# Kernel tuning notes

Hardware: AMD Instinct MI355X
Metric: run time of the kernel (lower is better)

The kernel has to match this reference:

```python
import jax, jax.numpy as jnp
import numpy as np

N = 5000      # nodes
E = 80000     # edges (avg degree 16)
B = 8         # batch of graph signals sharing one graph
IN = 30       # input feature dim (10 steps x 3)
H = 4         # attention heads
D = 64        # hidden dim per head
HD = H * D    # 256
OUT = 3       # output features per step
NUM_GAT_LAYERS = 4  # num_layer=5 -> 1 + (5-2) layers
EPS = 1e-5


def setup_inputs() -> dict:
    key = jax.random.key(0)
    ks = jax.random.split(key, 40)
    inp = {}
    inp["xx"] = jax.random.normal(ks[0], (B, N, IN), dtype=jnp.float32)
    inp["src"] = jax.random.randint(ks[1], (E,), 0, N, dtype=jnp.int32)
    inp["dst"] = jax.random.randint(ks[2], (E,), 0, N, dtype=jnp.int32)
    dims = [IN, HD, HD, HD]
    k = 3
    for l in range(NUM_GAT_LAYERS):
        fan_in = dims[l]
        inp[f"W{l}"] = jax.random.normal(ks[k], (fan_in, HD), dtype=jnp.float32) / np.sqrt(fan_in); k += 1
        inp[f"al{l}"] = jax.random.normal(ks[k], (H, D), dtype=jnp.float32) * 0.1; k += 1
        inp[f"ar{l}"] = jax.random.normal(ks[k], (H, D), dtype=jnp.float32) * 0.1; k += 1
        inp[f"gamma{l}"] = jnp.ones((HD,), dtype=jnp.float32)
        inp[f"beta{l}"] = jnp.zeros((HD,), dtype=jnp.float32)
    inp["W_out"] = jax.random.normal(ks[k], (HD, OUT), dtype=jnp.float32) / np.sqrt(HD); k += 1
    inp["b_out"] = jnp.zeros((OUT,), dtype=jnp.float32)
    inp["output_length"] = 5
    return inp


def _gat_conv(x, W, al, ar, src, dst):
    # DGL GATConv: fc -> per-head attn logits -> edge softmax over dst -> scatter-sum
    h = (x @ W).reshape(N, H, D)                       # [N,H,D]
    el = (h * al).sum(-1)                              # [N,H]
    er = (h * ar).sum(-1)                              # [N,H]
    e = jax.nn.leaky_relu(el[src] + er[dst], 0.2)      # [E,H]
    m = jax.ops.segment_max(e, dst, num_segments=N)    # [N,H] (stable softmax)
    ex = jnp.exp(e - m[dst])                           # [E,H]
    s = jax.ops.segment_sum(ex, dst, num_segments=N)   # [N,H]
    alpha = ex / s[dst]                                # [E,H]
    return jax.ops.segment_sum(alpha[:, :, None] * h[src], dst, num_segments=N)  # [N,H,D]


def _gat_layer(x, W, al, ar, gamma, beta, src, dst):
    # per-sample GATConv, flatten heads, BatchNorm1d (training stats) over (B,N), LeakyReLU
    out = jax.vmap(lambda xb: _gat_conv(xb, W, al, ar, src, dst))(x)  # [B,N,H,D]
    out = out.reshape(B, N, HD)
    mu = out.mean(axis=(0, 1))
    var = out.var(axis=(0, 1))  # biased, matches torch BN normalization
    out = (out - mu) * jax.lax.rsqrt(var + EPS) * gamma + beta
    return jax.nn.leaky_relu(out, 0.01)


def reference(xx, src, dst,
              W0, al0, ar0, gamma0, beta0,
              W1, al1, ar1, gamma1, beta1,
              W2, al2, ar2, gamma2, beta2,
              W3, al3, ar3, gamma3, beta3,
              W_out, b_out, output_length):
    layers = [(W0, al0, ar0, gamma0, beta0),
              (W1, al1, ar1, gamma1, beta1),
              (W2, al2, ar2, gamma2, beta2),
              (W3, al3, ar3, gamma3, beta3)]
    outputs = []
    for _ in range(output_length):
        h = xx
        for (W, al, ar, g, b) in layers:
            h = _gat_layer(h, W, al, ar, g, b, src, dst)
        out = h @ W_out + b_out                      # [B,N,OUT]
        xx = jnp.concatenate([xx[:, :, 3:], out], axis=-1)
        outputs.append(out[:, :, None, :])
    return jnp.concatenate(outputs, axis=2)          # [B,N,T,OUT]
```

## Files before the change

### kernel.cpp

```cpp
#include <hip/hip_runtime.h>
#include <math.h>

#define NNODES 5000
#define NEDGES 80000
#define NB 8
#define NIN 30
#define K0PAD 32
#define NH 4
#define ND 64
#define NHD 256
#define NT 5
#define NOUT 3
#define ROWS (NB * NNODES)
#define BNEPS 1e-5f
#define KP 40
#define NREP 8
#define BM 32

#define GLOBAL_AS __attribute__((address_space(1)))
#define LDS_AS __attribute__((address_space(3)))

typedef short shortx8 __attribute__((ext_vector_type(8)));
typedef _Float16 halfx8 __attribute__((ext_vector_type(8)));
typedef _Float16 halfx4 __attribute__((ext_vector_type(4)));
typedef _Float16 halfx2 __attribute__((ext_vector_type(2)));
typedef float floatx4 __attribute__((ext_vector_type(4)));

static __device__ __forceinline__ unsigned short f2h(float f) {
    union { _Float16 h; unsigned short u; } v;
    v.h = (_Float16)f;
    return v.u;
}
static __device__ __forceinline__ float h2f(unsigned short u) {
    union { _Float16 h; unsigned short u; } v;
    v.u = u;
    return (float)v.h;
}


__global__ void count_kernel(const int* __restrict__ dst, int* __restrict__ counts, int n) {
    int e = blockIdx.x * blockDim.x + threadIdx.x;
    if (e < n) atomicAdd(&counts[dst[e]], 1);
}

__global__ __launch_bounds__(1024) void scan_kernel(const int* __restrict__ counts,
                                                    int* __restrict__ offsets, int n) {
    __shared__ int smem[1024];
    const int CH = 5;
    int tid = threadIdx.x;
    int base = tid * CH;
    int loc[CH];
    int s = 0;
    for (int j = 0; j < CH; ++j) {
        int i = base + j;
        int v = (i < n) ? counts[i] : 0;
        loc[j] = s;
        s += v;
    }
    smem[tid] = s;
    __syncthreads();
    for (int off = 1; off < 1024; off <<= 1) {
        int v = (tid >= off) ? smem[tid - off] : 0;
        __syncthreads();
        smem[tid] += v;
        __syncthreads();
    }
    int excl = smem[tid] - s;
    for (int j = 0; j < CH; ++j) {
        int i = base + j;
        if (i < n) offsets[i] = excl + loc[j];
    }
    if (tid == 1023) offsets[n] = smem[1023];
}

__global__ void fill_kernel(const int* __restrict__ src, const int* __restrict__ dst,
                            const int* __restrict__ offsets, int* __restrict__ cursor,
                            int* __restrict__ csr_src, int n) {
    int e = blockIdx.x * blockDim.x + threadIdx.x;
    if (e >= n) return;
    int d = dst[e];
    int pos = offsets[d] + atomicAdd(&cursor[d], 1);
    csr_src[pos] = src[e];
}


__global__ void pack_xx_kernel(const float* __restrict__ xx, unsigned short* __restrict__ xx16) {
    int idx = blockIdx.x * blockDim.x + threadIdx.x;
    if (idx >= ROWS * K0PAD) return;
    int g = idx >> 5;
    int k = idx & 31;
    float v = (k < NIN) ? xx[(size_t)g * NIN + k] : 0.0f;
    xx16[idx] = f2h(v);
}

__global__ void packWt_kernel(const float* __restrict__ W0, const float* __restrict__ W1,
                              const float* __restrict__ W2, const float* __restrict__ W3,
                              unsigned short* __restrict__ P0, unsigned short* __restrict__ P1,
                              unsigned short* __restrict__ P2, unsigned short* __restrict__ P3) {
    int l = blockIdx.y;
    const float* W = (l == 0) ? W0 : (l == 1) ? W1 : (l == 2) ? W2 : W3;
    unsigned short* WtP = (l == 0) ? P0 : (l == 1) ? P1 : (l == 2) ? P2 : P3;
    int Kin = (l == 0) ? NIN : NHD;
    int Kpad = (l == 0) ? K0PAD : NHD;
    int n = blockIdx.x;
    int k = threadIdx.x;
    if (k < Kpad) {
        float v = (k < Kin) ? W[(size_t)k * NHD + n] : 0.0f;
        int t = k >> 5;
        int quad = (k >> 3) & 3;
        int j = k & 7;
        int p = n * 4 + (quad ^ ((n >> 1) & 3));
        WtP[(size_t)t * (NHD * 32) + p * 8 + j] = f2h(v);
    }
}


__global__ __launch_bounds__(256) void gemm_mfma_kernel(
    const unsigned short* __restrict__ A, const unsigned short* __restrict__ Wt,
    const float* __restrict__ alw, const float* __restrict__ arw,
    const float* __restrict__ sums, const float* __restrict__ gamma,
    const float* __restrict__ beta, int apply_bn,
    unsigned short* __restrict__ C16, float* __restrict__ el, float* __restrict__ er,
    int K) {
    __shared__ __align__(16) short As[BM * KP];
    __shared__ __align__(16) short Bs[256 * 32];
    __shared__ float bn_scale[NHD];
    __shared__ float bn_shift[NHD];
    int tid = threadIdx.x;
    if (apply_bn) {
        int c = tid;
        float s = 0.0f, s2 = 0.0f;
#pragma unroll
        for (int r2 = 0; r2 < NREP; ++r2) {
            s += sums[r2 * 2 * NHD + c];
            s2 += sums[r2 * 2 * NHD + NHD + c];
        }
        const float invn = 1.0f / (float)ROWS;
        float mu = s * invn;
        float var = s2 * invn - mu * mu;
        float sc = rsqrtf(var + BNEPS) * gamma[c];
        bn_scale[c] = sc;
        bn_shift[c] = beta[c] - mu * sc;
    }
    __syncthreads();

    int wave = tid >> 6;
    int lane = tid & 63;
    int c = lane & 15;
    int quad = lane >> 4;
    int xorv = (c >> 1) & 3;
    int row0 = blockIdx.x * BM;

    floatx4 acc[2][4];
#pragma unroll
    for (int mt = 0; mt < 2; ++mt)
#pragma unroll
        for (int nt = 0; nt < 4; ++nt) acc[mt][nt] = (floatx4){0.f, 0.f, 0.f, 0.f};

    int r = tid >> 2;
    int seg = tid & 3;
    for (int k0 = 0; k0 < K; k0 += 32) {
        const unsigned short* gB = Wt + (size_t)(k0 >> 5) * (NHD * 32);
#pragma unroll
        for (int i = 0; i < 4; ++i) {
            int ci = i * 256 + tid;
            __builtin_amdgcn_global_load_lds(
                (const GLOBAL_AS unsigned int*)(gB + ci * 8),
                (LDS_AS unsigned int*)(&Bs[ci * 8]), 16, 0, 0);
        }
        if (r < BM) {
            shortx8 v = *(const shortx8*)(A + (size_t)(row0 + r) * K + k0 + seg * 8);
            if (apply_bn) {
                halfx8 hv = *(halfx8*)&v;
                int kg = k0 + seg * 8;
#pragma unroll
                for (int j = 0; j < 8; ++j) {
                    float x = (float)hv[j];
                    x = fmaf(x, bn_scale[kg + j], bn_shift[kg + j]);
                    x = (x > 0.0f) ? x : 0.01f * x;
                    hv[j] = (_Float16)x;
                }
                v = *(shortx8*)&hv;
            }
            *(shortx8*)(&As[r * KP + seg * 8]) = v;
        }
        __syncthreads();
        halfx8 a[2], b[4];
#pragma unroll
        for (int mt = 0; mt < 2; ++mt)
            a[mt] = *(const halfx8*)(&As[(mt * 16 + c) * KP + quad * 8]);
#pragma unroll
        for (int nt = 0; nt < 4; ++nt) {
            int pq = (wave * 64 + nt * 16 + c) * 4 + (quad ^ xorv);
            b[nt] = *(const halfx8*)(&Bs[pq * 8]);
        }
#pragma unroll
        for (int mt = 0; mt < 2; ++mt)
#pragma unroll
            for (int nt = 0; nt < 4; ++nt)
                acc[mt][nt] = __builtin_amdgcn_mfma_f32_16x16x32_f16(a[mt], b[nt],
                                                                     acc[mt][nt], 0, 0, 0);
        __syncthreads();
    }

    float alv[4], arv[4];
#pragma unroll
    for (int nt = 0; nt < 4; ++nt) {
        alv[nt] = alw[wave * 64 + nt * 16 + c];
        arv[nt] = arw[wave * 64 + nt * 16 + c];
    }
#pragma unroll
    for (int mt = 0; mt < 2; ++mt) {
#pragma unroll
        for (int rr = 0; rr < 4; ++rr) {
            int row = row0 + mt * 16 + quad * 4 + rr;
            float pl = 0.0f, pr = 0.0f;
#pragma unroll
            for (int nt = 0; nt < 4; ++nt) {
                float v = acc[mt][nt][rr];
                C16[(size_t)row * NHD + wave * 64 + nt * 16 + c] = f2h(v);
                pl += v * alv[nt];
                pr += v * arv[nt];
            }
#pragma unroll
            for (int o = 1; o < 16; o <<= 1) {
                pl += __shfl_xor(pl, o);
                pr += __shfl_xor(pr, o);
            }
            if (c == mt * 4 + rr) {
                el[(size_t)row * NH + wave] = pl;
                er[(size_t)row * NH + wave] = pr;
            }
        }
    }
}


__global__ __launch_bounds__(256) void attn_kernel(const unsigned short* __restrict__ h16,
                                                   const float* __restrict__ el,
                                                   const float* __restrict__ er,
                                                   const int* __restrict__ offsets,
                                                   const int* __restrict__ csr_src,
                                                   unsigned short* __restrict__ out16,
                                                   float* __restrict__ sums) {
    int p = blockIdx.x;
    int tid = threadIdx.x;
    if (p == 0) {
        for (int i = tid; i < NREP * 2 * NHD; i += 256) sums[i] = 0.0f;
    }
    int b = p & 7;
    int wave = tid >> 6;
    int lane = tid & 63;
    int head = lane >> 4;
    int li = lane & 15;
    int n = ((p >> 3) << 2) + wave;
    int g = b * NNODES + n;
    int start = offsets[n];
    int deg = offsets[n + 1] - start;
    if (deg == 0) {
        *(unsigned long long*)(out16 + (size_t)g * NHD + lane * 4) = 0ULL;
        return;
    }
    const float* elb = el + (size_t)b * NNODES * NH;
    float er_nh = er[(size_t)g * NH + head];

    if (deg <= 64) {
        float e[4], w[4];
        int s[4];
#pragma unroll
        for (int k = 0; k < 4; ++k) {
            int idx = k * 16 + li;
            if (idx < deg) {
                s[k] = csr_src[start + idx];
                float t = elb[s[k] * NH + head] + er_nh;
                e[k] = (t > 0.0f) ? t : 0.2f * t;
            } else {
                s[k] = 0;
                e[k] = -INFINITY;
            }
        }
        float mx = fmaxf(fmaxf(e[0], e[1]), fmaxf(e[2], e[3]));
#pragma unroll
        for (int o = 8; o; o >>= 1) mx = fmaxf(mx, __shfl_xor(mx, o));
        float sm = 0.0f;
#pragma unroll
        for (int k = 0; k < 4; ++k) {
            w[k] = __expf(e[k] - mx);
            sm += w[k];
        }
#pragma unroll
        for (int o = 8; o; o >>= 1) sm += __shfl_xor(sm, o);

        int sub = lane >> 5;
        int i32 = lane & 31;
        int hsel = (lane & 24) << 1;
        float smh = __shfl(sm, hsel);
        const unsigned short* hrow = h16 + (size_t)b * NNODES * NHD + i32 * 8;
        float a0 = 0.f, a1 = 0.f, a2 = 0.f, a3 = 0.f;
        float a4 = 0.f, a5 = 0.f, a6 = 0.f, a7 = 0.f;
#define GATHER_CHUNK(K)                                                          \
        if (deg > (K) * 16) {                                                    \
            int cnt = deg - (K) * 16;                                            \
            cnt = (cnt > 16) ? 16 : cnt;                                         \
            int j = 0;                                                           \
            for (; j + 4 <= cnt; j += 4) {                                       \
                int sa = __shfl(s[K], j + sub);                                  \
                float wa = __shfl(w[K], hsel + j + sub);                         \
                int sb = __shfl(s[K], j + 2 + sub);                              \
                float wb = __shfl(w[K], hsel + j + 2 + sub);                     \
                halfx8 ha = *(const halfx8*)(hrow + (size_t)sa * NHD);           \
                halfx8 hb = *(const halfx8*)(hrow + (size_t)sb * NHD);           \
                a0 += wa * (float)ha[0]; a1 += wa * (float)ha[1];                \
                a2 += wa * (float)ha[2]; a3 += wa * (float)ha[3];                \
                a4 += wa * (float)ha[4]; a5 += wa * (float)ha[5];                \
                a6 += wa * (float)ha[6]; a7 += wa * (float)ha[7];                \
                a0 += wb * (float)hb[0]; a1 += wb * (float)hb[1];                \
                a2 += wb * (float)hb[2]; a3 += wb * (float)hb[3];                \
                a4 += wb * (float)hb[4]; a5 += wb * (float)hb[5];                \
                a6 += wb * (float)hb[6]; a7 += wb * (float)hb[7];                \
            }                                                                    \
            for (; j < cnt; j += 2) {                                            \
                int e2 = j + sub;                                                \
                bool valid = (e2 < cnt);                                         \
                int ec = valid ? e2 : (cnt - 1);                                 \
                int sa = __shfl(s[K], ec);                                       \
                float wa0 = __shfl(w[K], hsel + ec);                             \
                float wa = valid ? wa0 : 0.0f;                                   \
                halfx8 ha = *(const halfx8*)(hrow + (size_t)sa * NHD);           \
                a0 += wa * (float)ha[0]; a1 += wa * (float)ha[1];                \
                a2 += wa * (float)ha[2]; a3 += wa * (float)ha[3];                \
                a4 += wa * (float)ha[4]; a5 += wa * (float)ha[5];                \
                a6 += wa * (float)ha[6]; a7 += wa * (float)ha[7];                \
            }                                                                    \
        }
        GATHER_CHUNK(0)
        GATHER_CHUNK(1)
        GATHER_CHUNK(2)
        GATHER_CHUNK(3)
#undef GATHER_CHUNK
        a0 += __shfl_xor(a0, 32); a1 += __shfl_xor(a1, 32);
        a2 += __shfl_xor(a2, 32); a3 += __shfl_xor(a3, 32);
        a4 += __shfl_xor(a4, 32); a5 += __shfl_xor(a5, 32);
        a6 += __shfl_xor(a6, 32); a7 += __shfl_xor(a7, 32);
        if (sub == 0) {
            float inv = 1.0f / smh;
            halfx8 o8;
            o8[0] = (_Float16)(a0 * inv); o8[1] = (_Float16)(a1 * inv);
            o8[2] = (_Float16)(a2 * inv); o8[3] = (_Float16)(a3 * inv);
            o8[4] = (_Float16)(a4 * inv); o8[5] = (_Float16)(a5 * inv);
            o8[6] = (_Float16)(a6 * inv); o8[7] = (_Float16)(a7 * inv);
            *(halfx8*)(out16 + (size_t)g * NHD + i32 * 8) = o8;
        }
    } else {
        const unsigned short* hbase = h16 + (size_t)b * NNODES * NHD + lane * 4;
        float mx = -INFINITY;
        for (int i = li; i < deg; i += 16) {
            int s2 = csr_src[start + i];
            float t = elb[s2 * NH + head] + er_nh;
            t = (t > 0.0f) ? t : 0.2f * t;
            mx = fmaxf(mx, t);
        }
#pragma unroll
        for (int o = 8; o; o >>= 1) mx = fmaxf(mx, __shfl_xor(mx, o));
        float sm = 0.0f;
        for (int i = li; i < deg; i += 16) {
            int s2 = csr_src[start + i];
            float t = elb[s2 * NH + head] + er_nh;
            t = (t > 0.0f) ? t : 0.2f * t;
            sm += __expf(t - mx);
        }
#pragma unroll
        for (int o = 8; o; o >>= 1) sm += __shfl_xor(sm, o);
        float a0 = 0.f, a1 = 0.f, a2 = 0.f, a3 = 0.f;
        for (int j = 0; j < deg; ++j) {
            int s2 = csr_src[start + j];
            float t = elb[s2 * NH + head] + er_nh;
            t = (t > 0.0f) ? t : 0.2f * t;
            float wj = __expf(t - mx);
            halfx4 hv = *(const halfx4*)(hbase + (size_t)s2 * NHD);
            a0 += wj * (float)hv[0];
            a1 += wj * (float)hv[1];
            a2 += wj * (float)hv[2];
            a3 += wj * (float)hv[3];
        }
        float inv = 1.0f / sm;
        halfx4 o4;
        o4[0] = (_Float16)(a0 * inv);
        o4[1] = (_Float16)(a1 * inv);
        o4[2] = (_Float16)(a2 * inv);
        o4[3] = (_Float16)(a3 * inv);
        *(halfx4*)(out16 + (size_t)g * NHD + lane * 4) = o4;
    }
}


__global__ __launch_bounds__(128) void bnreduce_kernel(const unsigned short* __restrict__ x16,
                                                       float* __restrict__ sums) {
    int tid = threadIdx.x;
    int c2 = tid * 2;
    float sx = 0.f, sx2 = 0.f, sy = 0.f, sy2 = 0.f;
    for (int row = blockIdx.x; row < ROWS; row += gridDim.x) {
        halfx2 hv = *(const halfx2*)(x16 + (size_t)row * NHD + c2);
        float vx = (float)hv.x, vy = (float)hv.y;
        sx += vx;
        sx2 += vx * vx;
        sy += vy;
        sy2 += vy * vy;
    }
    float* sr = sums + (blockIdx.x & (NREP - 1)) * 2 * NHD;
    atomicAdd(&sr[c2], sx);
    atomicAdd(&sr[c2 + 1], sy);
    atomicAdd(&sr[NHD + c2], sx2);
    atomicAdd(&sr[NHD + c2 + 1], sy2);
}


__global__ __launch_bounds__(256) void headout_kernel(const unsigned short* __restrict__ x16,
                                                      const float* __restrict__ sums,
                                                      const float* __restrict__ gamma,
                                                      const float* __restrict__ beta,
                                                      const float* __restrict__ Wout,
                                                      const float* __restrict__ bout,
                                                      float* __restrict__ out,
                                                      unsigned short* __restrict__ xx16, int t) {
    __shared__ float bsc[NHD];
    __shared__ float bsh[NHD];
    {
        int c = threadIdx.x;
        float s = 0.0f, s2 = 0.0f;
#pragma unroll
        for (int r2 = 0; r2 < NREP; ++r2) {
            s += sums[r2 * 2 * NHD + c];
            s2 += sums[r2 * 2 * NHD + NHD + c];
        }
        const float invn = 1.0f / (float)ROWS;
        float mu = s * invn;
        float var = s2 * invn - mu * mu;
        float sc = rsqrtf(var + BNEPS) * gamma[c];
        bsc[c] = sc;
        bsh[c] = beta[c] - mu * sc;
    }
    __syncthreads();

    int wave = threadIdx.x >> 6;
    int lane = threadIdx.x & 63;
    int g = blockIdx.x * 4 + wave;
    int c0 = lane * 4;
    halfx4 hv = *(const halfx4*)(x16 + (size_t)g * NHD + c0);
    float vv[4];
#pragma unroll
    for (int j = 0; j < 4; ++j) {
        float x = fmaf((float)hv[j], bsc[c0 + j], bsh[c0 + j]);
        vv[j] = (x > 0.0f) ? x : 0.01f * x;
    }
    float r0 = vv[0] * Wout[(c0 + 0) * NOUT + 0] + vv[1] * Wout[(c0 + 1) * NOUT + 0] +
               vv[2] * Wout[(c0 + 2) * NOUT + 0] + vv[3] * Wout[(c0 + 3) * NOUT + 0];
    float r1 = vv[0] * Wout[(c0 + 0) * NOUT + 1] + vv[1] * Wout[(c0 + 1) * NOUT + 1] +
               vv[2] * Wout[(c0 + 2) * NOUT + 1] + vv[3] * Wout[(c0 + 3) * NOUT + 1];
    float r2 = vv[0] * Wout[(c0 + 0) * NOUT + 2] + vv[1] * Wout[(c0 + 1) * NOUT + 2] +
               vv[2] * Wout[(c0 + 2) * NOUT + 2] + vv[3] * Wout[(c0 + 3) * NOUT + 2];
#pragma unroll
    for (int o = 32; o; o >>= 1) {
        r0 += __shfl_xor(r0, o);
        r1 += __shfl_xor(r1, o);
        r2 += __shfl_xor(r2, o);
    }
    float o0 = r0 + bout[0], o1 = r1 + bout[1], o2 = r2 + bout[2];
    if (lane == 0) {
        float* op = out + ((size_t)g * NT + t) * NOUT;
        op[0] = o0;
        op[1] = o1;
        op[2] = o2;
    }
    float oldv = (lane < NIN) ? h2f(xx16[(size_t)g * K0PAD + lane]) : 0.0f;
    float shifted = __shfl(oldv, lane + 3);
    float newv = (lane < 27) ? shifted : (lane == 27 ? o0 : (lane == 28 ? o1 : o2));
    if (lane < NIN) xx16[(size_t)g * K0PAD + lane] = f2h(newv);
}


extern "C" void kernel_launch(void* const* d_in, const int* in_sizes, int n_in,
                              void* d_out, int out_size, void* d_ws, size_t ws_size,
                              hipStream_t stream) {
    const float* xx = (const float*)d_in[0];
    const int* src = (const int*)d_in[1];
    const int* dst = (const int*)d_in[2];
    const float* W[4] = {(const float*)d_in[3], (const float*)d_in[8],
                         (const float*)d_in[13], (const float*)d_in[18]};
    const float* al[4] = {(const float*)d_in[4], (const float*)d_in[9],
                          (const float*)d_in[14], (const float*)d_in[19]};
    const float* ar[4] = {(const float*)d_in[5], (const float*)d_in[10],
                          (const float*)d_in[15], (const float*)d_in[20]};
    const float* gamma[4] = {(const float*)d_in[6], (const float*)d_in[11],
                             (const float*)d_in[16], (const float*)d_in[21]};
    const float* beta[4] = {(const float*)d_in[7], (const float*)d_in[12],
                            (const float*)d_in[17], (const float*)d_in[22]};
    const float* W_out = (const float*)d_in[23];
    const float* b_out = (const float*)d_in[24];
    float* out = (float*)d_out;

    float* wsf = (float*)d_ws;
    float* el = wsf;
    float* er = el + (size_t)ROWS * NH;
    float* sums = er + (size_t)ROWS * NH;
    unsigned short* h16 = (unsigned short*)(sums + NREP * 2 * NHD);
    unsigned short* act16 = h16 + (size_t)ROWS * NHD;
    unsigned short* xx16 = act16 + (size_t)ROWS * NHD;
    unsigned short* Wt0 = xx16 + (size_t)ROWS * K0PAD;
    unsigned short* Wt1 = Wt0 + 256 * K0PAD;
    unsigned short* Wt2 = Wt1 + 256 * NHD;
    unsigned short* Wt3 = Wt2 + 256 * NHD;
    int* counts = (int*)(Wt3 + 256 * NHD);
    int* offsets = counts + NNODES;
    int* cursor = offsets + NNODES + 8;
    int* csr_src = cursor + NNODES;
    const unsigned short* Wt[4] = {Wt0, Wt1, Wt2, Wt3};

    hipMemsetAsync(counts, 0, NNODES * sizeof(int), stream);
    count_kernel<<<(NEDGES + 255) / 256, 256, 0, stream>>>(dst, counts, NEDGES);
    scan_kernel<<<1, 1024, 0, stream>>>(counts, offsets, NNODES);
    hipMemsetAsync(cursor, 0, NNODES * sizeof(int), stream);
    fill_kernel<<<(NEDGES + 255) / 256, 256, 0, stream>>>(src, dst, offsets, cursor,
                                                          csr_src, NEDGES);
    pack_xx_kernel<<<(ROWS * K0PAD + 255) / 256, 256, 0, stream>>>(xx, xx16);
    packWt_kernel<<<dim3(256, 4), 256, 0, stream>>>(W[0], W[1], W[2], W[3],
                                                    (unsigned short*)Wt0,
                                                    (unsigned short*)Wt1,
                                                    (unsigned short*)Wt2,
                                                    (unsigned short*)Wt3);

    for (int t = 0; t < NT; ++t) {
        for (int l = 0; l < 4; ++l) {
            const unsigned short* A16 = (l == 0) ? xx16 : act16;
            int K = (l == 0) ? K0PAD : NHD;
            int apply_bn = (l > 0) ? 1 : 0;
            const float* pg = gamma[(l > 0) ? l - 1 : 0];
            const float* pb = beta[(l > 0) ? l - 1 : 0];
            gemm_mfma_kernel<<<ROWS / BM, 256, 0, stream>>>(A16, Wt[l], al[l], ar[l],
                                                            sums, pg, pb, apply_bn,
                                                            h16, el, er, K);
            attn_kernel<<<ROWS / 4, 256, 0, stream>>>(h16, el, er, offsets, csr_src,
                                                      act16, sums);
            bnreduce_kernel<<<640, 128, 0, stream>>>(act16, sums);
        }
        headout_kernel<<<ROWS / 4, 256, 0, stream>>>(act16, sums, gamma[3], beta[3],
                                                     W_out, b_out, out, xx16, t);
    }
}
```

Before: 1.511 ms.

## Fuse BatchNorm statistics reduction into attention kernel with double-buffered sums

Removes the separate bnreduce kernel by having each attention block reduce per-channel sum and sum-of-squares of its outputs in LDS and atomically add them into replicated global accumulators. Sums buffers are double-buffered so the next GEMM can zero the current buffer while reading the previous one, and the replica count is raised to spread atomics. This avoids re-reading the activation tensor and one launch per layer, at the cost of many more global atomics and an extra LDS sync per block.

```diff
diff --git a/kernel.cpp b/kernel.cpp
--- a/kernel.cpp
+++ b/kernel.cpp
@@ -14,7 +14,7 @@
 #define ROWS (NB * NNODES)
 #define BNEPS 1e-5f
 #define KP 40
-#define NREP 8
+#define NREP 64
 #define BM 32
 
 #define GLOBAL_AS __attribute__((address_space(1)))
@@ -118,8 +118,8 @@
 __global__ __launch_bounds__(256) void gemm_mfma_kernel(
     const unsigned short* __restrict__ A, const unsigned short* __restrict__ Wt,
     const float* __restrict__ alw, const float* __restrict__ arw,
-    const float* __restrict__ sums, const float* __restrict__ gamma,
-    const float* __restrict__ beta, int apply_bn,
+    const float* __restrict__ sums_read, float* __restrict__ sums_zero,
+    const float* __restrict__ gamma, const float* __restrict__ beta, int apply_bn,
     unsigned short* __restrict__ C16, float* __restrict__ el, float* __restrict__ er,
     int K) {
     __shared__ __align__(16) short As[BM * KP];
@@ -127,13 +127,16 @@
     __shared__ float bn_scale[NHD];
     __shared__ float bn_shift[NHD];
     int tid = threadIdx.x;
+    {
+        int zi = blockIdx.x * 256 + tid;
+        if (zi < NREP * 2 * NHD) sums_zero[zi] = 0.0f;
+    }
     if (apply_bn) {
         int c = tid;
         float s = 0.0f, s2 = 0.0f;
-#pragma unroll
         for (int r2 = 0; r2 < NREP; ++r2) {
-            s += sums[r2 * 2 * NHD + c];
-            s2 += sums[r2 * 2 * NHD + NHD + c];
+            s += sums_read[r2 * 2 * NHD + c];
+            s2 += sums_read[r2 * 2 * NHD + NHD + c];
         }
         const float invn = 1.0f / (float)ROWS;
         float mu = s * invn;
@@ -242,12 +245,10 @@
                                                    const int* __restrict__ offsets,
                                                    const int* __restrict__ csr_src,
                                                    unsigned short* __restrict__ out16,
-                                                   float* __restrict__ sums) {
+                                                   float* __restrict__ sums_cur) {
+    __shared__ float bnpart[4][2][NHD];
     int p = blockIdx.x;
     int tid = threadIdx.x;
-    if (p == 0) {
-        for (int i = tid; i < NREP * 2 * NHD; i += 256) sums[i] = 0.0f;
-    }
     int b = p & 7;
     int wave = tid >> 6;
     int lane = tid & 63;
@@ -257,14 +258,19 @@
     int g = b * NNODES + n;
     int start = offsets[n];
     int deg = offsets[n + 1] - start;
+    const float* elb = el + (size_t)b * NNODES * NH;
+    float er_nh = er[(size_t)g * NH + head];
+    float* bw = &bnpart[wave][0][0];
+
     if (deg == 0) {
         *(unsigned long long*)(out16 + (size_t)g * NHD + lane * 4) = 0ULL;
-        return;
-    }
-    const float* elb = el + (size_t)b * NNODES * NH;
-    float er_nh = er[(size_t)g * NH + head];
-
-    if (deg <= 64) {
+        int c4 = lane * 4;
+#pragma unroll
+        for (int j = 0; j < 4; ++j) {
+            bw[c4 + j] = 0.0f;
+            bw[NHD + c4 + j] = 0.0f;
+        }
+    } else if (deg <= 64) {
         float e[4], w[4];
         int s[4];
 #pragma unroll
@@ -350,6 +356,13 @@
             o8[4] = (_Float16)(a4 * inv); o8[5] = (_Float16)(a5 * inv);
             o8[6] = (_Float16)(a6 * inv); o8[7] = (_Float16)(a7 * inv);
             *(halfx8*)(out16 + (size_t)g * NHD + i32 * 8) = o8;
+            int c8 = i32 * 8;
+#pragma unroll
+            for (int j = 0; j < 8; ++j) {
+                float v = (float)o8[j];
+                bw[c8 + j] = v;
+                bw[NHD + c8 + j] = v * v;
+            }
         }
     } else {
         const unsigned short* hbase = h16 + (size_t)b * NNODES * NHD + lane * 4;
@@ -390,28 +403,23 @@
         o4[2] = (_Float16)(a2 * inv);
         o4[3] = (_Float16)(a3 * inv);
         *(halfx4*)(out16 + (size_t)g * NHD + lane * 4) = o4;
-    }
-}
-
-
-__global__ __launch_bounds__(128) void bnreduce_kernel(const unsigned short* __restrict__ x16,
-                                                       float* __restrict__ sums) {
-    int tid = threadIdx.x;
-    int c2 = tid * 2;
-    float sx = 0.f, sx2 = 0.f, sy = 0.f, sy2 = 0.f;
-    for (int row = blockIdx.x; row < ROWS; row += gridDim.x) {
-        halfx2 hv = *(const halfx2*)(x16 + (size_t)row * NHD + c2);
-        float vx = (float)hv.x, vy = (float)hv.y;
-        sx += vx;
-        sx2 += vx * vx;
-        sy += vy;
-        sy2 += vy * vy;
-    }
-    float* sr = sums + (blockIdx.x & (NREP - 1)) * 2 * NHD;
-    atomicAdd(&sr[c2], sx);
-    atomicAdd(&sr[c2 + 1], sy);
-    atomicAdd(&sr[NHD + c2], sx2);
-    atomicAdd(&sr[NHD + c2 + 1], sy2);
+        int c4 = lane * 4;
+#pragma unroll
+        for (int j = 0; j < 4; ++j) {
+            float v = (float)o4[j];
+            bw[c4 + j] = v;
+            bw[NHD + c4 + j] = v * v;
+        }
+    }
+    __syncthreads();
+    {
+        int c = tid;
+        float s = bnpart[0][0][c] + bnpart[1][0][c] + bnpart[2][0][c] + bnpart[3][0][c];
+        float s2 = bnpart[0][1][c] + bnpart[1][1][c] + bnpart[2][1][c] + bnpart[3][1][c];
+        float* sr = sums_cur + (p & (NREP - 1)) * 2 * NHD;
+        atomicAdd(&sr[c], s);
+        atomicAdd(&sr[NHD + c], s2);
+    }
 }
 
 
@@ -428,7 +436,6 @@
     {
         int c = threadIdx.x;
         float s = 0.0f, s2 = 0.0f;
-#pragma unroll
         for (int r2 = 0; r2 < NREP; ++r2) {
             s += sums[r2 * 2 * NHD + c];
             s2 += sums[r2 * 2 * NHD + NHD + c];
@@ -502,8 +509,9 @@
     float* wsf = (float*)d_ws;
     float* el = wsf;
     float* er = el + (size_t)ROWS * NH;
-    float* sums = er + (size_t)ROWS * NH;
-    unsigned short* h16 = (unsigned short*)(sums + NREP * 2 * NHD);
+    float* sumsA = er + (size_t)ROWS * NH;
+    float* sumsB = sumsA + NREP * 2 * NHD;
+    unsigned short* h16 = (unsigned short*)(sumsB + NREP * 2 * NHD);
     unsigned short* act16 = h16 + (size_t)ROWS * NHD;
     unsigned short* xx16 = act16 + (size_t)ROWS * NHD;
     unsigned short* Wt0 = xx16 + (size_t)ROWS * K0PAD;
@@ -529,6 +537,7 @@
                                                     (unsigned short*)Wt2,
                                                     (unsigned short*)Wt3);
 
+    int idx = 0;
     for (int t = 0; t < NT; ++t) {
         for (int l = 0; l < 4; ++l) {
             const unsigned short* A16 = (l == 0) ? xx16 : act16;
@@ -536,14 +545,16 @@
             int apply_bn = (l > 0) ? 1 : 0;
             const float* pg = gamma[(l > 0) ? l - 1 : 0];
             const float* pb = beta[(l > 0) ? l - 1 : 0];
+            float* cur = (idx & 1) ? sumsB : sumsA;
+            const float* prev = (idx & 1) ? sumsA : sumsB;
             gemm_mfma_kernel<<<ROWS / BM, 256, 0, stream>>>(A16, Wt[l], al[l], ar[l],
-                                                            sums, pg, pb, apply_bn,
+                                                            prev, cur, pg, pb, apply_bn,
                                                             h16, el, er, K);
             attn_kernel<<<ROWS / 4, 256, 0, stream>>>(h16, el, er, offsets, csr_src,
-                                                      act16, sums);
-            bnreduce_kernel<<<640, 128, 0, stream>>>(act16, sums);
-        }
-        headout_kernel<<<ROWS / 4, 256, 0, stream>>>(act16, sums, gamma[3], beta[3],
+                                                      act16, cur);
+            ++idx;
+        }
+        headout_kernel<<<ROWS / 4, 256, 0, stream>>>(act16, sumsB, gamma[3], beta[3],
                                                      W_out, b_out, out, xx16, t);
     }
 }
```

After: 1.527 ms. About the same (+1.1%).
